# Performance work log

Measured on AMD Instinct MI355X. Metric: run time of the kernel, lower is better.

## Reference

```python
import jax, jax.numpy as jnp
import numpy as np

B, C, H, W = 32, 384, 32, 32
NCH = 4           # chunks per branch (mixing_size = [4,4,4])
CH = C // NCH     # 96 channels per chunk


def setup_inputs() -> dict:
    key = jax.random.key(0)
    ks = iter(jax.random.split(key, 32))
    r = lambda shape, s=0.05: jax.random.normal(next(ks), shape, dtype=jnp.float32) * s
    inp = {"x": jax.random.normal(next(ks), (B, C, H, W), dtype=jnp.float32)}
    for b, k in zip((1, 2, 3), (1, 3, 5)):
        inp[f"f{b}_mlp_w1"] = r((2, CH, CH // 8))
        inp[f"f{b}_mlp_b1"] = r((2, CH // 8))
        inp[f"f{b}_mlp_w2"] = r((2, CH // 8, CH))
        inp[f"f{b}_mlp_b2"] = r((2, CH))
        inp[f"f{b}_conv_w"] = r((2, CH, 1, k, k))
        inp[f"f{b}_conv_b"] = r((2, CH))
    inp["fusion_w1"] = r((C, C // 4))
    inp["fusion_b1"] = r((C // 4,))
    inp["fusion_w2"] = r((C // 4, 3 * C))
    inp["fusion_b2"] = r((3 * C,))
    inp["proj_w"] = r((C, C))
    inp["proj_b"] = r((C,))
    return inp


def _gelu(x):
    return jax.nn.gelu(x, approximate=False)  # torch nn.GELU default (erf)


def _branch(x, mw1, mb1, mw2, mb2, cw, cb, pad):
    # x: (B, C, H, W); chunks of CH channels; even idx -> MLP (channel-last), odd -> depthwise conv
    chunks = jnp.split(x, NCH, axis=1)
    outs, mi, ci = [], 0, 0
    for i, c in enumerate(chunks):
        if i % 2 == 0:
            h = _gelu(jnp.einsum('bchw,cd->bdhw', c, mw1[mi]) + mb1[mi][:, None, None])
            y = jnp.einsum('bdhw,dc->bchw', h, mw2[mi]) + mb2[mi][:, None, None]
            mi += 1
        else:
            y = jax.lax.conv_general_dilated(
                c, cw[ci], window_strides=(1, 1), padding=[(pad, pad), (pad, pad)],
                feature_group_count=CH, dimension_numbers=('NCHW', 'OIHW', 'NCHW'))
            y = y + cb[ci][:, None, None]
            ci += 1
        outs.append(y)
    return jnp.concatenate(outs, axis=1)


def reference(x,
              f1_mlp_w1, f1_mlp_b1, f1_mlp_w2, f1_mlp_b2, f1_conv_w, f1_conv_b,
              f2_mlp_w1, f2_mlp_b1, f2_mlp_w2, f2_mlp_b2, f2_conv_w, f2_conv_b,
              f3_mlp_w1, f3_mlp_b1, f3_mlp_w2, f3_mlp_b2, f3_conv_w, f3_conv_b,
              fusion_w1, fusion_b1, fusion_w2, fusion_b2, proj_w, proj_b):
    x1 = _branch(x, f1_mlp_w1, f1_mlp_b1, f1_mlp_w2, f1_mlp_b2, f1_conv_w, f1_conv_b, pad=0)
    x2 = _branch(x, f2_mlp_w1, f2_mlp_b1, f2_mlp_w2, f2_mlp_b2, f2_conv_w, f2_conv_b, pad=1)
    x3 = _branch(x, f3_mlp_w1, f3_mlp_b1, f3_mlp_w2, f3_mlp_b2, f3_conv_w, f3_conv_b, pad=2)
    # softmax-gated multi-scale fusion
    a = (x1 + x2 + x3).mean(axis=(2, 3))                            # (B, C)
    g = _gelu(a @ fusion_w1 + fusion_b1) @ fusion_w2 + fusion_b2     # (B, 3C)
    g = g.reshape(a.shape[0], C, 3).transpose(2, 0, 1)               # (3, B, C)
    w = jax.nn.softmax(g, axis=0)[:, :, :, None, None]               # (3, B, C, 1, 1)
    comb = x1 * w[0] + x2 * w[1] + x3 * w[2]                         # (B, C, H, W)
    out = jnp.einsum('bchw,cd->bdhw', comb, proj_w) + proj_b[:, None, None]
    return out
```

## Files before the change

kernel.cpp:

```cpp
#include <hip/hip_runtime.h>
#include <math.h>

#define B_  32
#define C_  384
#define HW  1024

typedef float          f32x4 __attribute__((ext_vector_type(4)));
typedef short          s16x8 __attribute__((ext_vector_type(8)));
typedef unsigned short us8v  __attribute__((ext_vector_type(8)));

struct KParams {
  const float* x;
  const float* mw1[3]; const float* mb1[3]; const float* mw2[3]; const float* mb2[3];
  const float* cw[3];  const float* cb[3];
  const float* fw1; const float* fb1; const float* fw2; const float* fb2;
  const float* pw;  const float* pb;
  float* wg;
  float* H_part;
  float* cvA;
  float* ext;
  unsigned short* pwT;
  float* out;
};

__device__ __forceinline__ float gelu_exact(float v) {
  return 0.5f * v * (1.0f + erff(v * 0.70710678118654752440f));
}
__device__ __forceinline__ unsigned short f2bf(float f) {
  unsigned u = __float_as_uint(f);
  u += 0x7FFFu + ((u >> 16) & 1u);
  return (unsigned short)(u >> 16);
}
__device__ __forceinline__ float bf2f(unsigned short h) {
  return __uint_as_float(((unsigned)h) << 16);
}

__global__ __launch_bounds__(256) void k_prep(KParams P) {
  __shared__ float tile[32][33];
  const int td = blockIdx.x % 12, tc = blockIdx.x / 12;
  const int j = threadIdx.x & 31, i0 = threadIdx.x >> 5;
  const int gcoff = (tc < 3) ? 0 : (tc < 6 ? 96 : (tc < 9 ? -96 : 0));
  for (int i = i0; i < 32; i += 8)
    tile[i][j] = P.pw[(size_t)(tc*32 + i + gcoff)*C_ + td*32 + j];
  __syncthreads();
  for (int i = i0; i < 32; i += 8)
    P.pwT[(size_t)(td*32 + i)*C_ + tc*32 + j] = f2bf(tile[j][i]);
}

template<int HALF>
__device__ __forceinline__ void conv_strip(const float* xc, int h0, int row,
                                           float w1t, const float* w3, const float* w5,
                                           float* y0, float* y1, float* y2) {
#pragma unroll
  for (int p = 0; p < 16; ++p) { y0[p] = 0.f; y1[p] = 0.f; y2[p] = 0.f; }
#pragma unroll
  for (int dy = 0; dy < 5; ++dy) {
    const int hr = h0 + row - 2 + dy;
    float win[20];
    if (hr >= 0 && hr < 32) {
#pragma unroll
      for (int u = 0; u < 5; ++u)
        *(float4*)&win[u*4] = *(const float4*)&xc[hr*32 + HALF*12 + u*4];
    } else {
#pragma unroll
      for (int u = 0; u < 20; ++u) win[u] = 0.f;
    }
#pragma unroll
    for (int dx = 0; dx < 5; ++dx) {
      const float w = w5[dy*5 + dx];
#pragma unroll
      for (int p = 0; p < 16; ++p) {
        const int ri = p + dx - 2 + HALF*4;
        if (ri >= 0 && ri < 20) y2[p] += win[ri] * w;
      }
    }
    if (dy >= 1 && dy <= 3) {
#pragma unroll
      for (int dx = 0; dx < 3; ++dx) {
        const float w = w3[(dy-1)*3 + dx];
#pragma unroll
        for (int p = 0; p < 16; ++p) {
          const int ri = p + dx - 1 + HALF*4;
          if (ri >= 0 && ri < 20) y1[p] += win[ri] * w;
        }
      }
      if (dy == 2) {
#pragma unroll
        for (int p = 0; p < 16; ++p) y0[p] = win[p + HALF*4] * w1t;
      }
    }
  }
}

__global__ __launch_bounds__(256, 2) void k_sum(KParams P) {
  __shared__ __align__(16) char sm[49152 + 13824 + 256];
  const int bid = blockIdx.x;
  const int b = bid >> 5, sub = bid & 31;
  const int t = threadIdx.x;

  if (sub < 16) {
    const int mi = sub >> 3, q = sub & 7;
    const int h0 = q * 4;
    float* Xl  = (float*)sm;
    float* w1l = (float*)(sm + 49152);
    float* Hl  = (float*)(sm + 49152 + 13824);
    for (int i = t; i < 3456; i += 256) {
      int s = i / 1152, r = i - s*1152;
      w1l[i] = P.mw1[s][mi*1152 + r];
    }
    for (int i = t*4; i < 12288; i += 1024) {
      int c = i >> 7, pix = i & 127;
      *(float4*)&Xl[i] = *(const float4*)&P.x[(size_t)(b*C_ + mi*192 + c)*HW + h0*32 + pix];
    }
    __syncthreads();
    const int quad = t & 31, sjg = t >> 6;
    const int cq = (t >> 5) & 1;
    const int sj0 = sjg * 9;
    float h[9][4];
#pragma unroll
    for (int u = 0; u < 9; ++u) { h[u][0]=0.f; h[u][1]=0.f; h[u][2]=0.f; h[u][3]=0.f; }
    int wbase[9];
#pragma unroll
    for (int u = 0; u < 9; ++u) {
      int sj = sj0 + u, s = sj / 12, jj = sj % 12;
      wbase[u] = s*1152 + jj;
    }
    for (int c = cq*48; c < cq*48 + 48; ++c) {
      const float4 xv = *(const float4*)&Xl[c*128 + quad*4];
#pragma unroll
      for (int u = 0; u < 9; ++u) {
        const float w = w1l[wbase[u] + c*12];
        h[u][0] += xv.x*w; h[u][1] += xv.y*w; h[u][2] += xv.z*w; h[u][3] += xv.w*w;
      }
    }
#pragma unroll
    for (int u = 0; u < 9; ++u)
#pragma unroll
      for (int p = 0; p < 4; ++p) h[u][p] += __shfl_xor(h[u][p], 32, 64);
    float hs[9];
#pragma unroll
    for (int u = 0; u < 9; ++u) {
      int sj = sj0 + u, s = sj / 12, jj = sj % 12;
      const float bias = P.mb1[s][mi*12 + jj];
      float sum = 0.f;
#pragma unroll
      for (int p = 0; p < 4; ++p) sum += gelu_exact(h[u][p] + bias);
#pragma unroll
      for (int m = 16; m >= 1; m >>= 1) sum += __shfl_xor(sum, m, 64);
      hs[u] = sum;
    }
    if ((t & 63) == 0) {
#pragma unroll
      for (int u = 0; u < 9; ++u) Hl[sj0 + u] = hs[u];
    }
    __syncthreads();
    if (t < 36) P.H_part[(size_t)((b*2 + mi)*8 + q)*36 + t] = Hl[t];
  } else {
    const int s2 = sub - 16;
    const int gi = s2 >> 3, q = s2 & 7;
    const int h0 = q * 4;
    const int lane = t & 63, wv = t >> 6;
    const int gcbase = (2*gi + 1) * 96;
    for (int i = 0; i < 24; ++i) {
      const int cc = wv*24 + i;
      const float* xc = P.x + (size_t)(b*C_ + gcbase + cc)*HW + h0*32;
      const float2 v = *(const float2*)(xc + 2*lane);
      const float t2 = v.x + v.y;
      float T = t2;
      T += __shfl_xor(T, 1, 64);  T += __shfl_xor(T, 2, 64);
      T += __shfl_xor(T, 4, 64);  T += __shfl_xor(T, 8, 64);
      T += __shfl_xor(T, 16, 64); T += __shfl_xor(T, 32, 64);
      float c0  = ((lane & 15) == 0)  ? v.x : 0.f;
      float c1  = ((lane & 15) == 0)  ? v.y : 0.f;
      float c30 = ((lane & 15) == 15) ? v.x : 0.f;
      float c31 = ((lane & 15) == 15) ? v.y : 0.f;
      c0  += __shfl_xor(c0, 16, 64);  c0  += __shfl_xor(c0, 32, 64);
      c1  += __shfl_xor(c1, 16, 64);  c1  += __shfl_xor(c1, 32, 64);
      c30 += __shfl_xor(c30, 16, 64); c30 += __shfl_xor(c30, 32, 64);
      c31 += __shfl_xor(c31, 16, 64); c31 += __shfl_xor(c31, 32, 64);
      if (lane == 0) {
        float* A = &P.cvA[(size_t)(b*2 + gi)*5*96 + cc];
        atomicAdd(A + 0*96, T);   atomicAdd(A + 1*96, c0);
        atomicAdd(A + 2*96, c1);  atomicAdd(A + 3*96, c30);
        atomicAdd(A + 4*96, c31);
      }
      if (q == 0 || q == 7) {
        float r = t2;
        r += __shfl_xor(r, 1, 64); r += __shfl_xor(r, 2, 64);
        r += __shfl_xor(r, 4, 64); r += __shfl_xor(r, 8, 64);
        const int e  = (q == 0) ? 0 : 1;
        const int lo = (q == 0) ? 0 : 32;
        const float Ra  = __shfl(r,   lo,      64), Rb  = __shfl(r,   lo + 16, 64);
        const float p00 = __shfl(v.x, lo,      64), p01 = __shfl(v.y, lo,      64);
        const float p0a = __shfl(v.x, lo + 15, 64), p0b = __shfl(v.y, lo + 15, 64);
        const float p10 = __shfl(v.x, lo + 16, 64), p11 = __shfl(v.y, lo + 16, 64);
        const float p1a = __shfl(v.x, lo + 31, 64), p1b = __shfl(v.y, lo + 31, 64);
        if (lane == 0) {
          float* E = &P.ext[((size_t)(b*2 + gi)*2 + e)*10*96 + cc];
          E[0*96] = Ra;  E[1*96] = Rb;
          E[2*96] = p00; E[3*96] = p01; E[4*96] = p0a; E[5*96] = p0b;
          E[6*96] = p10; E[7*96] = p11; E[8*96] = p1a; E[9*96] = p1b;
        }
      }
    }
  }
}

__global__ __launch_bounds__(256) void k_gate(KParams P) {
  const int b = blockIdx.x, t = threadIdx.x;
  __shared__ float am[C_], g1p[2][96], g1v[96], Hs[2][36];
  for (int i = t; i < 72; i += 256) {
    int mi = i / 36, sj = i % 36;
    float s = 0.f;
    for (int q = 0; q < 8; ++q) s += P.H_part[(size_t)((b*2+mi)*8 + q)*36 + sj];
    Hs[mi][sj] = s * (1.0f/1024.0f);
  }
  __syncthreads();
  for (int i = t; i < 192; i += 256) {
    int mi = i / 96, cc = i % 96;
    float a = 0.f;
    for (int s = 0; s < 3; ++s) {
      float y = P.mb2[s][mi*96 + cc];
      for (int jj = 0; jj < 12; ++jj) y += Hs[mi][s*12+jj] * P.mw2[s][mi*1152 + jj*96 + cc];
      a += y;
    }
    am[mi*192 + cc] = a;
  }
  for (int i = t; i < 192; i += 256) {
    const int gi = i / 96, cc = i % 96;
    const float* A  = &P.cvA[(size_t)(b*2 + gi)*5*96 + cc];
    const float T   = A[0*96];
    const float C0  = A[1*96], C1  = A[2*96], C30 = A[3*96], C31 = A[4*96];
    const float* E0 = &P.ext[((size_t)(b*2 + gi)*2 + 0)*10*96 + cc];
    const float* E1 = &P.ext[((size_t)(b*2 + gi)*2 + 1)*10*96 + cc];
    const float R0  = E0[0*96], R1  = E0[1*96];
    const float a00 = E0[2*96], a01 = E0[3*96], a0a = E0[4*96], a0b = E0[5*96];
    const float a10 = E0[6*96], a11 = E0[7*96], a1a = E0[8*96], a1b = E0[9*96];
    const float R30 = E1[0*96], R31 = E1[1*96];
    const float b00 = E1[2*96], b01 = E1[3*96], b0a = E1[4*96], b0b = E1[5*96];
    const float b10 = E1[6*96], b11 = E1[7*96], b1a = E1[8*96], b1b = E1[9*96];
    const float ER[5]   = {R30+R31, R31, 0.f, R0, R0+R1};
    const float EC[5]   = {C30+C31, C31, 0.f, C0, C0+C1};
    const float cr0[5]  = {a0a+a0b, a0b, 0.f, a00, a00+a01};
    const float cr1[5]  = {a1a+a1b, a1b, 0.f, a10, a10+a11};
    const float cr30[5] = {b0a+b0b, b0b, 0.f, b00, b00+b01};
    const float cr31[5] = {b1a+b1b, b1b, 0.f, b10, b10+b11};
    const int gcl = gi*96 + cc;
    float sum = P.cw[0][gcl] * T;
#pragma unroll
    for (int dy = 0; dy < 3; ++dy)
#pragma unroll
      for (int dx = 0; dx < 3; ++dx) {
        const int s = dy - 1, u = dx - 1;
        float xc_ = 0.f;
        if (s == 1)  xc_ = cr0[u+2];
        if (s == -1) xc_ = cr31[u+2];
        sum += P.cw[1][gcl*9 + dy*3 + dx] * (T - ER[s+2] - EC[u+2] + xc_);
      }
#pragma unroll
    for (int dy = 0; dy < 5; ++dy)
#pragma unroll
      for (int dx = 0; dx < 5; ++dx) {
        const int s = dy - 2, u = dx - 2;
        float xc_ = 0.f;
        if (s == 1)  xc_ = cr0[u+2];
        if (s == 2)  xc_ = cr0[u+2] + cr1[u+2];
        if (s == -1) xc_ = cr31[u+2];
        if (s == -2) xc_ = cr30[u+2] + cr31[u+2];
        sum += P.cw[2][gcl*25 + dy*5 + dx] * (T - ER[s+2] - EC[u+2] + xc_);
      }
    am[(2*gi+1)*96 + cc] = sum * (1.0f/1024.0f)
                         + P.cb[0][gcl] + P.cb[1][gcl] + P.cb[2][gcl];
  }
  __syncthreads();
  if (t < 192) {
    const int jj = t % 96, half = t / 96;
    float acc = 0.f;
    for (int c = half*192; c < half*192 + 192; ++c) acc += am[c] * P.fw1[c*96 + jj];
    g1p[half][jj] = acc;
  }
  __syncthreads();
  if (t < 96) g1v[t] = gelu_exact(g1p[0][t] + g1p[1][t] + P.fb1[t]);
  __syncthreads();
  for (int c = t; c < C_; c += 256) {
    float l0 = P.fb2[c*3+0], l1 = P.fb2[c*3+1], l2 = P.fb2[c*3+2];
    for (int jj = 0; jj < 96; ++jj) {
      const float g = g1v[jj];
      const float* f = P.fw2 + jj*1152 + c*3;
      l0 += g*f[0]; l1 += g*f[1]; l2 += g*f[2];
    }
    const float m = fmaxf(l0, fmaxf(l1, l2));
    const float e0 = expf(l0-m), e1 = expf(l1-m), e2 = expf(l2-m);
    const float inv = 1.0f/(e0+e1+e2);
    P.wg[0*(B_*C_) + b*C_ + c] = e0*inv;
    P.wg[1*(B_*C_) + b*C_ + c] = e1*inv;
    P.wg[2*(B_*C_) + b*C_ + c] = e2*inv;
  }
}

template<int HALF>
__device__ __forceinline__ void conv_phase2(const KParams& P, int b, int h0,
                                            char* combB, const float* wgl, int tt) {
  for (int it = 0; it < 2; ++it) {
    const int task = tt + 512*it;
    if (task < 768) {
      const int row = task & 3, c192 = task >> 2;
      const int gi = c192 / 96, cc = c192 - gi*96;
      const int gcl = gi*96 + cc;
      const int gc = (2*gi + 1)*96 + cc;
      const int kp = 192 + gi*96 + cc;
      const float* xc = P.x + (size_t)(b*C_ + gc)*HW;
      const float w1t = P.cw[0][gcl];
      float w3[9], w5[25];
#pragma unroll
      for (int k2 = 0; k2 < 9; ++k2)  w3[k2] = P.cw[1][gcl*9 + k2];
#pragma unroll
      for (int k2 = 0; k2 < 25; ++k2) w5[k2] = P.cw[2][gcl*25 + k2];
      float y0[16], y1[16], y2[16];
      conv_strip<HALF>(xc, h0, row, w1t, w3, w5, y0, y1, y2);
      const float g0 = wgl[0*C_ + gc], g1 = wgl[1*C_ + gc], g2 = wgl[2*C_ + gc];
      const float cbg = g0*P.cb[0][gcl] + g1*P.cb[1][gcl] + g2*P.cb[2][gcl];
#pragma unroll
      for (int p = 0; p < 16; ++p) {
        const float v = g0*y0[p] + g1*y1[p] + g2*y2[p] + cbg;
        const int pix = row*32 + HALF*16 + p;
        const int off = pix*768 + ((kp*2) ^ ((pix & 15) << 4));
        *(unsigned short*)(combB + off) = f2bf(v);
      }
    }
  }
}

__global__ __launch_bounds__(1024) void k_proj(KParams P) {
  __shared__ __align__(16) char smem[159744];
  char* combB = smem;
  char* hlB   = smem + 98304;
  char* XB    = smem + 116736;
  unsigned short* wlB = (unsigned short*)(smem + 141312);
  float* wgl  = (float*)(smem + 155136);

  const int t  = threadIdx.x;
  const int b  = blockIdx.x >> 3;
  const int h0 = (blockIdx.x & 7) * 4;

  for (int i = t; i < 1152; i += 1024)
    wgl[i] = P.wg[(size_t)(i/C_)*(B_*C_) + b*C_ + (i % C_)];
  for (int i = t; i < 6912; i += 1024) {
    int s = i / 2304, r = i - s*2304, mi2 = r / 1152, rr = r - mi2*1152;
    wlB[i] = f2bf(P.mw1[s][mi2*1152 + rr]);
  }
  for (int i = t*4; i < 12288; i += 4096) {
    int c = i >> 7, pix = i & 127;
    float4 v = *(const float4*)&P.x[(size_t)(b*C_ + c)*HW + h0*32 + pix];
    unsigned lo = (unsigned)f2bf(v.x) | ((unsigned)f2bf(v.y) << 16);
    unsigned hi = (unsigned)f2bf(v.z) | ((unsigned)f2bf(v.w) << 16);
    *(uint2*)(XB + c*256 + pix*2) = make_uint2(lo, hi);
  }
  __syncthreads();

#pragma unroll 1
  for (int mi = 0; mi < 2; ++mi) {
    if (t < 512) {
      const int oct = t & 15, cq = (t >> 4) & 3, sjg = t >> 6;
      const int nsj = (sjg < 4) ? 5 : 4;
      const int sj0 = (sjg < 4) ? sjg*5 : 20 + (sjg - 4)*4;
      int wbase[5]; float bias[5];
#pragma unroll
      for (int u = 0; u < 5; ++u) {
        int sj = sj0 + ((u < nsj) ? u : 0);
        int s = sj / 12, jj = sj - s*12;
        wbase[u] = (s*2 + mi)*1152 + jj;
        bias[u] = P.mb1[s][mi*12 + jj];
      }
      float h[5][8];
#pragma unroll
      for (int u = 0; u < 5; ++u)
#pragma unroll
        for (int p = 0; p < 8; ++p) h[u][p] = 0.f;
      for (int c = cq*24; c < cq*24 + 24; ++c) {
        const us8v xv = *(const us8v*)(XB + c*256 + oct*16);
        float xf[8];
#pragma unroll
        for (int p = 0; p < 8; ++p) xf[p] = bf2f(xv[p]);
#pragma unroll
        for (int u = 0; u < 5; ++u) {
          if (u < nsj) {
            const float w = bf2f(wlB[wbase[u] + c*12]);
#pragma unroll
            for (int p = 0; p < 8; ++p) h[u][p] += xf[p]*w;
          }
        }
      }
#pragma unroll
      for (int u = 0; u < 5; ++u)
#pragma unroll
        for (int p = 0; p < 8; ++p) {
          h[u][p] += __shfl_xor(h[u][p], 16, 64);
          h[u][p] += __shfl_xor(h[u][p], 32, 64);
        }
      if (cq == 0) {
#pragma unroll
        for (int u = 0; u < 5; ++u) {
          if (u < nsj) {
            us8v o;
#pragma unroll
            for (int p = 0; p < 8; ++p) o[p] = f2bf(gelu_exact(h[u][p] + bias[u]));
            *(us8v*)(hlB + (mi*36 + sj0 + u)*256 + oct*16) = o;
          }
        }
      }
    } else {
      if (mi == 0) conv_phase2<0>(P, b, h0, combB, wgl, t - 512);
      else         conv_phase2<1>(P, b, h0, combB, wgl, t - 512);
    }
    __syncthreads();
    if (mi == 0) {
      for (int i = t*4; i < 12288; i += 4096) {
        int c = i >> 7, pix = i & 127;
        float4 v = *(const float4*)&P.x[(size_t)(b*C_ + 192 + c)*HW + h0*32 + pix];
        unsigned lo = (unsigned)f2bf(v.x) | ((unsigned)f2bf(v.y) << 16);
        unsigned hi = (unsigned)f2bf(v.z) | ((unsigned)f2bf(v.w) << 16);
        *(uint2*)(XB + c*256 + pix*2) = make_uint2(lo, hi);
      }
      __syncthreads();
    }
  }

  for (int i = t; i < 6912; i += 1024) {
    int s = i / 2304, r = i - s*2304, mi2 = r / 1152, rr = r - mi2*1152;
    wlB[i] = f2bf(P.mw2[s][mi2*1152 + rr]);
  }
  __syncthreads();

  {
    const int ct = t & 31, pt = (t >> 5) & 15, mi = t >> 9;
    const int c0 = ct*3, pix0 = pt*8;
    float wgc[3][3];
#pragma unroll
    for (int s = 0; s < 3; ++s)
#pragma unroll
      for (int i = 0; i < 3; ++i) wgc[s][i] = wgl[s*C_ + mi*192 + c0 + i];
    float acc[3][8];
#pragma unroll
    for (int i = 0; i < 3; ++i) {
      float ai = 0.f;
#pragma unroll
      for (int s = 0; s < 3; ++s) ai += wgc[s][i] * P.mb2[s][mi*96 + c0 + i];
#pragma unroll
      for (int p = 0; p < 8; ++p) acc[i][p] = ai;
    }
#pragma unroll
    for (int s = 0; s < 3; ++s)
#pragma unroll
      for (int jj = 0; jj < 12; ++jj) {
        const us8v hv = *(const us8v*)(hlB + (mi*36 + s*12 + jj)*256 + pix0*2);
        float hf[8];
#pragma unroll
        for (int p = 0; p < 8; ++p) hf[p] = bf2f(hv[p]);
        const unsigned short* wp = wlB + (s*2 + mi)*1152 + jj*96 + c0;
        float gw[3];
#pragma unroll
        for (int i = 0; i < 3; ++i) gw[i] = bf2f(wp[i]) * wgc[s][i];
#pragma unroll
        for (int i = 0; i < 3; ++i)
#pragma unroll
          for (int p = 0; p < 8; ++p) acc[i][p] += gw[i]*hf[p];
      }
#pragma unroll
    for (int i = 0; i < 3; ++i)
#pragma unroll
      for (int p = 0; p < 8; ++p) {
        const int pix = pix0 + p;
        const int kp2 = mi*96 + c0 + i;
        const int off = pix*768 + ((kp2*2) ^ ((pix & 15) << 4));
        *(unsigned short*)(combB + off) = f2bf(acc[i][p]);
      }
  }
  __syncthreads();

  {
    const int lane = t & 63, wv = t >> 6;
    const int wm = wv & 1, wn = wv >> 1;
    const int l15 = lane & 15, l4 = lane >> 4;
    f32x4 acc[4][3];
#pragma unroll
    for (int mt = 0; mt < 4; ++mt)
#pragma unroll
      for (int nt = 0; nt < 3; ++nt) acc[mt][nt] = (f32x4){0.f,0.f,0.f,0.f};
    const char* pwTb = (const char*)P.pwT;
#pragma unroll 2
    for (int ks = 0; ks < 12; ++ks) {
      const int k0 = ks*32 + l4*8;
      s16x8 af[4], bfr[3];
#pragma unroll
      for (int mt = 0; mt < 4; ++mt) {
        const int m = wm*64 + mt*16 + l15;
        af[mt] = *(const s16x8*)(combB + m*768 + ((2*k0) ^ ((m & 15) << 4)));
      }
#pragma unroll
      for (int nt = 0; nt < 3; ++nt) {
        const int d = wn*48 + nt*16 + l15;
        bfr[nt] = *(const s16x8*)(pwTb + (size_t)d*768 + 2*k0);
      }
#pragma unroll
      for (int mt = 0; mt < 4; ++mt)
#pragma unroll
        for (int nt = 0; nt < 3; ++nt)
          acc[mt][nt] = __builtin_amdgcn_mfma_f32_16x16x32_bf16(af[mt], bfr[nt], acc[mt][nt], 0, 0, 0);
    }
#pragma unroll
    for (int nt = 0; nt < 3; ++nt) {
      const int d = wn*48 + nt*16 + l15;
      const float pbv = P.pb[d];
#pragma unroll
      for (int mt = 0; mt < 4; ++mt) {
        const int pix = wm*64 + mt*16 + l4*4;
        float4 o;
        o.x = acc[mt][nt][0] + pbv;
        o.y = acc[mt][nt][1] + pbv;
        o.z = acc[mt][nt][2] + pbv;
        o.w = acc[mt][nt][3] + pbv;
        *(float4*)&P.out[(size_t)(b*C_ + d)*HW + (h0 + (pix >> 5))*32 + (pix & 31)] = o;
      }
    }
  }
}

extern "C" void kernel_launch(void* const* d_in, const int* in_sizes, int n_in,
                              void* d_out, int out_size, void* d_ws, size_t ws_size,
                              hipStream_t stream) {
  KParams P;
  P.x = (const float*)d_in[0];
  for (int s = 0; s < 3; ++s) {
    const int base = 1 + s * 6;
    P.mw1[s] = (const float*)d_in[base + 0];
    P.mb1[s] = (const float*)d_in[base + 1];
    P.mw2[s] = (const float*)d_in[base + 2];
    P.mb2[s] = (const float*)d_in[base + 3];
    P.cw[s]  = (const float*)d_in[base + 4];
    P.cb[s]  = (const float*)d_in[base + 5];
  }
  P.fw1 = (const float*)d_in[19]; P.fb1 = (const float*)d_in[20];
  P.fw2 = (const float*)d_in[21]; P.fb2 = (const float*)d_in[22];
  P.pw  = (const float*)d_in[23]; P.pb  = (const float*)d_in[24];
  float* w = (float*)d_ws;
  P.wg     = w;
  P.H_part = w + 36864;
  P.cvA    = w + 55296;
  P.ext    = w + 86016;
  P.pwT    = (unsigned short*)(w + 208896);
  P.out = (float*)d_out;

  hipMemsetAsync((char*)d_ws + 55296*sizeof(float), 0, 30720*sizeof(float), stream);
  k_prep<<<144, 256, 0, stream>>>(P);
  k_sum <<<1024, 256, 0, stream>>>(P);
  k_gate<<<32, 256, 0, stream>>>(P);
  k_proj<<<256, 1024, 0, stream>>>(P);
}
```

Measured before the change: 304.9 us.

## Merge prep into sum kernel, widen gate, restructure proj MLP and swizzle

Folds the proj-weight transpose/bf16 conversion into the main reduction kernel as extra blocks, which removes one launch. The gate kernel moves to 512 threads so the MLP mean and conv mean run concurrently and the fusion matmul splits four ways. In k_proj, the first MLP layer is rewritten so each lane owns two pixels and reads vectorised weight rows from a transposed layout, dropping the cross-lane shuffle reduction. Also changes the LDS swizzle to mix higher pixel bits, remaps block order across batches, and adds an occupancy hint. These touch several independent costs, and the new loop does more per-thread work with less parallelism over channels.

```diff
diff --git a/kernel.cpp b/kernel.cpp
--- a/kernel.cpp
+++ b/kernel.cpp
@@ -8,6 +8,8 @@
 typedef float          f32x4 __attribute__((ext_vector_type(4)));
 typedef short          s16x8 __attribute__((ext_vector_type(8)));
 typedef unsigned short us8v  __attribute__((ext_vector_type(8)));
+
+#define SWZ(pix) ((((pix) ^ ((pix) >> 4)) & 15) << 4)
 
 struct KParams {
   const float* x;
@@ -35,18 +37,6 @@
   return __uint_as_float(((unsigned)h) << 16);
 }
 
-__global__ __launch_bounds__(256) void k_prep(KParams P) {
-  __shared__ float tile[32][33];
-  const int td = blockIdx.x % 12, tc = blockIdx.x / 12;
-  const int j = threadIdx.x & 31, i0 = threadIdx.x >> 5;
-  const int gcoff = (tc < 3) ? 0 : (tc < 6 ? 96 : (tc < 9 ? -96 : 0));
-  for (int i = i0; i < 32; i += 8)
-    tile[i][j] = P.pw[(size_t)(tc*32 + i + gcoff)*C_ + td*32 + j];
-  __syncthreads();
-  for (int i = i0; i < 32; i += 8)
-    P.pwT[(size_t)(td*32 + i)*C_ + tc*32 + j] = f2bf(tile[j][i]);
-}
-
 template<int HALF>
 __device__ __forceinline__ void conv_strip(const float* xc, int h0, int row,
                                            float w1t, const float* w3, const float* w5,
@@ -92,12 +82,26 @@
   }
 }
 
-__global__ __launch_bounds__(256, 2) void k_sum(KParams P) {
+__global__ __launch_bounds__(256, 2) void k_work(KParams P) {
   __shared__ __align__(16) char sm[49152 + 13824 + 256];
   const int bid = blockIdx.x;
+  const int t = threadIdx.x;
+
+  if (bid >= 1024) {
+    const int pbk = bid - 1024;
+    float (*tile)[33] = (float(*)[33])sm;
+    const int td = pbk % 12, tc = pbk / 12;
+    const int j = t & 31, i0 = t >> 5;
+    const int gcoff = (tc < 3) ? 0 : (tc < 6 ? 96 : (tc < 9 ? -96 : 0));
+    for (int i = i0; i < 32; i += 8)
+      tile[i][j] = P.pw[(size_t)(tc*32 + i + gcoff)*C_ + td*32 + j];
+    __syncthreads();
+    for (int i = i0; i < 32; i += 8)
+      P.pwT[(size_t)(td*32 + i)*C_ + tc*32 + j] = f2bf(tile[j][i]);
+    return;
+  }
+
   const int b = bid >> 5, sub = bid & 31;
-  const int t = threadIdx.x;
-
   if (sub < 16) {
     const int mi = sub >> 3, q = sub & 7;
     const int h0 = q * 4;
@@ -206,18 +210,18 @@
   }
 }
 
-__global__ __launch_bounds__(256) void k_gate(KParams P) {
+__global__ __launch_bounds__(512) void k_gate(KParams P) {
   const int b = blockIdx.x, t = threadIdx.x;
-  __shared__ float am[C_], g1p[2][96], g1v[96], Hs[2][36];
-  for (int i = t; i < 72; i += 256) {
+  __shared__ float am[C_], g1p[4][96], g1v[96], Hs[2][36];
+  for (int i = t; i < 72; i += 512) {
     int mi = i / 36, sj = i % 36;
     float s = 0.f;
     for (int q = 0; q < 8; ++q) s += P.H_part[(size_t)((b*2+mi)*8 + q)*36 + sj];
     Hs[mi][sj] = s * (1.0f/1024.0f);
   }
   __syncthreads();
-  for (int i = t; i < 192; i += 256) {
-    int mi = i / 96, cc = i % 96;
+  if (t < 192) {
+    const int mi = t / 96, cc = t % 96;
     float a = 0.f;
     for (int s = 0; s < 3; ++s) {
       float y = P.mb2[s][mi*96 + cc];
@@ -225,8 +229,8 @@
       a += y;
     }
     am[mi*192 + cc] = a;
-  }
-  for (int i = t; i < 192; i += 256) {
+  } else if (t < 384) {
+    const int i = t - 192;
     const int gi = i / 96, cc = i % 96;
     const float* A  = &P.cvA[(size_t)(b*2 + gi)*5*96 + cc];
     const float T   = A[0*96];
@@ -273,16 +277,17 @@
                          + P.cb[0][gcl] + P.cb[1][gcl] + P.cb[2][gcl];
   }
   __syncthreads();
-  if (t < 192) {
-    const int jj = t % 96, half = t / 96;
+  if (t < 384) {
+    const int quarter = t / 96, jj = t % 96;
     float acc = 0.f;
-    for (int c = half*192; c < half*192 + 192; ++c) acc += am[c] * P.fw1[c*96 + jj];
-    g1p[half][jj] = acc;
-  }
-  __syncthreads();
-  if (t < 96) g1v[t] = gelu_exact(g1p[0][t] + g1p[1][t] + P.fb1[t]);
-  __syncthreads();
-  for (int c = t; c < C_; c += 256) {
+    for (int c = quarter*96; c < quarter*96 + 96; ++c) acc += am[c] * P.fw1[c*96 + jj];
+    g1p[quarter][jj] = acc;
+  }
+  __syncthreads();
+  if (t < 96) g1v[t] = gelu_exact(g1p[0][t] + g1p[1][t] + g1p[2][t] + g1p[3][t] + P.fb1[t]);
+  __syncthreads();
+  if (t < 384) {
+    const int c = t;
     float l0 = P.fb2[c*3+0], l1 = P.fb2[c*3+1], l2 = P.fb2[c*3+2];
     for (int jj = 0; jj < 96; ++jj) {
       const float g = g1v[jj];
@@ -324,14 +329,14 @@
       for (int p = 0; p < 16; ++p) {
         const float v = g0*y0[p] + g1*y1[p] + g2*y2[p] + cbg;
         const int pix = row*32 + HALF*16 + p;
-        const int off = pix*768 + ((kp*2) ^ ((pix & 15) << 4));
+        const int off = pix*768 + ((kp*2) ^ SWZ(pix));
         *(unsigned short*)(combB + off) = f2bf(v);
       }
     }
   }
 }
 
-__global__ __launch_bounds__(1024) void k_proj(KParams P) {
+__global__ __launch_bounds__(1024, 4) void k_proj(KParams P) {
   __shared__ __align__(16) char smem[159744];
   char* combB = smem;
   char* hlB   = smem + 98304;
@@ -340,14 +345,16 @@
   float* wgl  = (float*)(smem + 155136);
 
   const int t  = threadIdx.x;
-  const int b  = blockIdx.x >> 3;
-  const int h0 = (blockIdx.x & 7) * 4;
+  const int rb = (blockIdx.x & 7) * 32 + (blockIdx.x >> 3);
+  const int b  = rb >> 3;
+  const int h0 = (rb & 7) * 4;
 
   for (int i = t; i < 1152; i += 1024)
     wgl[i] = P.wg[(size_t)(i/C_)*(B_*C_) + b*C_ + (i % C_)];
   for (int i = t; i < 6912; i += 1024) {
     int s = i / 2304, r = i - s*2304, mi2 = r / 1152, rr = r - mi2*1152;
-    wlB[i] = f2bf(P.mw1[s][mi2*1152 + rr]);
+    int c = rr / 12, jj = rr - c*12;
+    wlB[(s*2 + mi2)*1152 + jj*96 + c] = f2bf(P.mw1[s][mi2*1152 + rr]);
   }
   for (int i = t*4; i < 12288; i += 4096) {
     int c = i >> 7, pix = i & 127;
@@ -361,52 +368,45 @@
 #pragma unroll 1
   for (int mi = 0; mi < 2; ++mi) {
     if (t < 512) {
-      const int oct = t & 15, cq = (t >> 4) & 3, sjg = t >> 6;
-      const int nsj = (sjg < 4) ? 5 : 4;
-      const int sj0 = (sjg < 4) ? sjg*5 : 20 + (sjg - 4)*4;
+      const int w = t >> 6, l = t & 63;
+      const int nsj = (w < 4) ? 5 : 4;
+      const int sj0 = (w < 4) ? w*5 : 20 + (w - 4)*4;
       int wbase[5]; float bias[5];
 #pragma unroll
       for (int u = 0; u < 5; ++u) {
         int sj = sj0 + ((u < nsj) ? u : 0);
         int s = sj / 12, jj = sj - s*12;
-        wbase[u] = (s*2 + mi)*1152 + jj;
+        wbase[u] = (s*2 + mi)*1152 + jj*96;
         bias[u] = P.mb1[s][mi*12 + jj];
       }
-      float h[5][8];
-#pragma unroll
-      for (int u = 0; u < 5; ++u)
-#pragma unroll
-        for (int p = 0; p < 8; ++p) h[u][p] = 0.f;
-      for (int c = cq*24; c < cq*24 + 24; ++c) {
-        const us8v xv = *(const us8v*)(XB + c*256 + oct*16);
-        float xf[8];
-#pragma unroll
-        for (int p = 0; p < 8; ++p) xf[p] = bf2f(xv[p]);
-#pragma unroll
-        for (int u = 0; u < 5; ++u) {
-          if (u < nsj) {
-            const float w = bf2f(wlB[wbase[u] + c*12]);
-#pragma unroll
-            for (int p = 0; p < 8; ++p) h[u][p] += xf[p]*w;
+      float h[5][2];
+#pragma unroll
+      for (int u = 0; u < 5; ++u) { h[u][0] = 0.f; h[u][1] = 0.f; }
+      for (int c0 = 0; c0 < 96; c0 += 8) {
+        us8v wv8[5];
+#pragma unroll
+        for (int u = 0; u < 5; ++u)
+          wv8[u] = *(const us8v*)(wlB + wbase[u] + c0);
+#pragma unroll
+        for (int cc = 0; cc < 8; ++cc) {
+          const unsigned xp = *(const unsigned*)(XB + (c0 + cc)*256 + l*4);
+          const float x0 = __uint_as_float(xp << 16);
+          const float x1 = __uint_as_float(xp & 0xFFFF0000u);
+#pragma unroll
+          for (int u = 0; u < 5; ++u) {
+            if (u < nsj) {
+              const float wv = bf2f(wv8[u][cc]);
+              h[u][0] += x0*wv; h[u][1] += x1*wv;
+            }
           }
         }
       }
 #pragma unroll
-      for (int u = 0; u < 5; ++u)
-#pragma unroll
-        for (int p = 0; p < 8; ++p) {
-          h[u][p] += __shfl_xor(h[u][p], 16, 64);
-          h[u][p] += __shfl_xor(h[u][p], 32, 64);
-        }
-      if (cq == 0) {
-#pragma unroll
-        for (int u = 0; u < 5; ++u) {
-          if (u < nsj) {
-            us8v o;
-#pragma unroll
-            for (int p = 0; p < 8; ++p) o[p] = f2bf(gelu_exact(h[u][p] + bias[u]));
-            *(us8v*)(hlB + (mi*36 + sj0 + u)*256 + oct*16) = o;
-          }
+      for (int u = 0; u < 5; ++u) {
+        if (u < nsj) {
+          const unsigned o = (unsigned)f2bf(gelu_exact(h[u][0] + bias[u]))
+                           | ((unsigned)f2bf(gelu_exact(h[u][1] + bias[u])) << 16);
+          *(unsigned*)(hlB + (mi*36 + sj0 + u)*256 + l*4) = o;
         }
       }
     } else {
@@ -428,7 +428,7 @@
 
   for (int i = t; i < 6912; i += 1024) {
     int s = i / 2304, r = i - s*2304, mi2 = r / 1152, rr = r - mi2*1152;
-    wlB[i] = f2bf(P.mw2[s][mi2*1152 + rr]);
+    wlB[(s*2 + mi2)*1152 + rr] = f2bf(P.mw2[s][mi2*1152 + rr]);
   }
   __syncthreads();
 
@@ -472,7 +472,7 @@
       for (int p = 0; p < 8; ++p) {
         const int pix = pix0 + p;
         const int kp2 = mi*96 + c0 + i;
-        const int off = pix*768 + ((kp2*2) ^ ((pix & 15) << 4));
+        const int off = pix*768 + ((kp2*2) ^ SWZ(pix));
         *(unsigned short*)(combB + off) = f2bf(acc[i][p]);
       }
   }
@@ -495,7 +495,7 @@
 #pragma unroll
       for (int mt = 0; mt < 4; ++mt) {
         const int m = wm*64 + mt*16 + l15;
-        af[mt] = *(const s16x8*)(combB + m*768 + ((2*k0) ^ ((m & 15) << 4)));
+        af[mt] = *(const s16x8*)(combB + m*768 + ((2*k0) ^ SWZ(m)));
       }
 #pragma unroll
       for (int nt = 0; nt < 3; ++nt) {
@@ -552,8 +552,7 @@
   P.out = (float*)d_out;
 
   hipMemsetAsync((char*)d_ws + 55296*sizeof(float), 0, 30720*sizeof(float), stream);
-  k_prep<<<144, 256, 0, stream>>>(P);
-  k_sum <<<1024, 256, 0, stream>>>(P);
-  k_gate<<<32, 256, 0, stream>>>(P);
+  k_work<<<1168, 256, 0, stream>>>(P);
+  k_gate<<<32, 512, 0, stream>>>(P);
   k_proj<<<256, 1024, 0, stream>>>(P);
 }
```

Result: faster. 289.8 us (-4.9%).
